# Performance work log

Measured on AMD Instinct MI355X. Metric: run time of the kernel, lower is better.

Reference implementation:

```python
import jax, jax.numpy as jnp
import numpy as np

B, S, HID = 1, 2048, 4096
NH, NKV, HD = 32, 8, 128
N_REP = NH // NKV
SCALING = HD ** -0.5
NEG_INF = jnp.float32(-jnp.inf)


def rotate_half(x):
    x1, x2 = jnp.split(x, 2, axis=-1)
    return jnp.concatenate((-x2, x1), axis=-1)


def setup_inputs() -> dict:
    key = jax.random.key(0)
    ks = jax.random.split(key, 8)
    hidden_states = jax.random.normal(ks[0], (B, S, HID), dtype=jnp.float32)
    # RoPE tables (uniform stand-ins; real cos/sin come from rotary embedding)
    pos = jnp.arange(S, dtype=jnp.float32)[:, None]
    inv_freq = 1.0 / (10000.0 ** (jnp.arange(0, HD, 2, dtype=jnp.float32) / HD))
    ang = pos * inv_freq[None, :]              # [S, HD/2]
    emb = jnp.concatenate([ang, ang], axis=-1)  # [S, HD]
    cos = jnp.cos(emb)[None].repeat(B, axis=0)  # [B, S, HD]
    sin = jnp.sin(emb)[None].repeat(B, axis=0)
    # HF-style additive causal mask: 0 on/below diagonal, -inf above
    tril = jnp.tril(jnp.ones((S, S), dtype=bool))
    attention_mask = jnp.where(tril, 0.0, NEG_INF).astype(jnp.float32)[None, None]  # [B,1,S,S]
    scale = 0.02
    q_w = jax.random.normal(ks[1], (HID, HID), dtype=jnp.float32) * scale
    k_w = jax.random.normal(ks[2], (NKV * HD, HID), dtype=jnp.float32) * scale
    v_w = jax.random.normal(ks[3], (NKV * HD, HID), dtype=jnp.float32) * scale
    o_w = jax.random.normal(ks[4], (HID, HID), dtype=jnp.float32) * scale
    return {"hidden_states": hidden_states, "cos": cos, "sin": sin,
            "attention_mask": attention_mask, "q_w": q_w, "k_w": k_w,
            "v_w": v_w, "o_w": o_w}


def reference(hidden_states, cos, sin, attention_mask, q_w, k_w, v_w, o_w):
    b, s, _ = hidden_states.shape
    # projections -> [B, H, S, D]
    q = (hidden_states @ q_w.T).reshape(b, s, NH, HD).transpose(0, 2, 1, 3)
    k = (hidden_states @ k_w.T).reshape(b, s, NKV, HD).transpose(0, 2, 1, 3)
    v = (hidden_states @ v_w.T).reshape(b, s, NKV, HD).transpose(0, 2, 1, 3)
    # RoPE (unsqueeze_dim=1)
    cos_u = cos[:, None, :, :]
    sin_u = sin[:, None, :, :]
    q = q * cos_u + rotate_half(q) * sin_u
    k = k * cos_u + rotate_half(k) * sin_u
    # repeat_kv (interleave each kv head n_rep times)
    k = jnp.repeat(k, N_REP, axis=1)
    v = jnp.repeat(v, N_REP, axis=1)
    attn = jnp.einsum("bhqd,bhkd->bhqk", q, k)
    # gen_mask: 0 -> 1, -inf -> 0 (passthrough otherwise)
    m = attention_mask
    mask01 = jnp.where(m == 0, 1.0, jnp.where(jnp.isneginf(m), 0.0, m))
    attn = attn * mask01
    causal = m[:, :, :, : k.shape[-2]]
    attn = (attn + causal) * SCALING
    probs = jax.nn.softmax(attn.astype(jnp.float32), axis=-1).astype(q.dtype)
    # dropout p=attention_dropout=0.0 in eval -> identity
    ctx = jnp.einsum("bhqk,bhkd->bhqd", probs, v)  # [B,H,S,D]
    out = ctx.transpose(0, 2, 1, 3).reshape(b, s, -1) @ o_w.T
    return out
```

## Files before the change

### kernel.cpp

```cpp
#include <hip/hip_runtime.h>


typedef __attribute__((ext_vector_type(8))) short bf16x8;
typedef __attribute__((ext_vector_type(4))) float f32x4;
typedef __attribute__((ext_vector_type(4))) unsigned short u16x4;

#define S_LEN 2048
#define HID 4096
#define NH 32
#define NKV 8
#define HD 128
#define KVDIM 1024
#define SCALING 0.08838834764831845f
#define ASC 0.12751744f
#define THR2 11.5415603f

__device__ inline unsigned short f2bf(float f) {
  unsigned u = __builtin_bit_cast(unsigned, f);
  u = (u + 0x7FFFu + ((u >> 16) & 1u)) >> 16;
  return (unsigned short)u;
}
__device__ inline unsigned short f2bf_fast(float f) {
  unsigned u = __builtin_bit_cast(unsigned, f);
  return (unsigned short)((u + 0x8000u) >> 16);
}
__device__ inline float bf2f(unsigned short h) {
  unsigned u = ((unsigned)h) << 16;
  return __builtin_bit_cast(float, u);
}

__device__ inline void gload_lds16(const unsigned short* g, unsigned short* l) {
  __builtin_amdgcn_global_load_lds(
      (const __attribute__((address_space(1))) void*)g,
      (__attribute__((address_space(3))) void*)l, 16, 0, 0);
}

#define SZ_HS (8388608u)
#define SZ_QW (16777216u)
#define SZ_KW (4194304u)
#define B0 SZ_HS
#define B1 (B0 + SZ_QW)
#define B2 (B1 + SZ_KW)
#define B3 (B2 + SZ_KW)
#define B4 (B3 + SZ_QW)

__global__ void cvt_all(const float* __restrict__ s0,
                        const float* __restrict__ s1,
                        const float* __restrict__ s2,
                        const float* __restrict__ s3,
                        const float* __restrict__ s4,
                        unsigned short* __restrict__ dst) {
  size_t i = ((size_t)blockIdx.x * blockDim.x + threadIdx.x) * 4;
  const float* src;
  size_t off;
  if (i < B0)      { src = s0; off = i; }
  else if (i < B1) { src = s1; off = i - B0; }
  else if (i < B2) { src = s2; off = i - B1; }
  else if (i < B3) { src = s3; off = i - B2; }
  else             { src = s4; off = i - B3; }
  f32x4 v = *(const f32x4*)(src + off);
  u16x4 o;
#pragma unroll
  for (int r = 0; r < 4; ++r) o[r] = f2bf(v[r]);
  *(u16x4*)(dst + i) = o;
}

__device__ inline const unsigned short* swz_src(const unsigned short* base,
                                                int s, int K) {
  const int g = s >> 3, q = s & 7, ls = q ^ (g & 7);
  return base + (size_t)(2 * g + (ls >> 2)) * K + (ls & 3) * 8;
}

__global__ __launch_bounds__(256, 3) void gemm_qkv(
    const unsigned short* __restrict__ A, const unsigned short* __restrict__ Bq_,
    const unsigned short* __restrict__ Bk_, const unsigned short* __restrict__ Bv_,
    const float* __restrict__ cosb, const float* __restrict__ sinb,
    unsigned short* __restrict__ Cq, unsigned short* __restrict__ Ck,
    unsigned short* __restrict__ Cvt) {
  __shared__ unsigned short As[2][128 * 32];
  __shared__ unsigned short Bs[2][128 * 32];
  const int K = HID;
  const int tid = threadIdx.x;
  const int lane = tid & 63;
  const int wave = tid >> 6;
  const int orig = blockIdx.y * gridDim.x + blockIdx.x;
  const int xcd = orig & 7, seq = orig >> 3;
  const int xt = xcd * ((int)gridDim.x >> 3) + (seq >> 4);
  const int yt = seq & 15;
  const int m0 = yt * 128;
  const int wr = wave >> 1, wc = wave & 1;
  const int lrow = lane & 15, lg = lane >> 4;

  const unsigned short* Bsel;
  if (xt < 32)      Bsel = Bq_ + (size_t)(xt * 128) * K;
  else if (xt < 40) Bsel = Bk_ + (size_t)((xt - 32) * 128) * K;
  else              Bsel = Bv_ + (size_t)((xt - 40) * 128) * K;

  const f32x4 zero = {0.f, 0.f, 0.f, 0.f};
  f32x4 acc[4][4];
#pragma unroll
  for (int i = 0; i < 4; ++i)
#pragma unroll
    for (int j = 0; j < 4; ++j) acc[i][j] = zero;

  const unsigned short* Ag0 = swz_src(A + (size_t)m0 * K, tid, K);
  const unsigned short* Ag1 = swz_src(A + (size_t)m0 * K, tid + 256, K);
  const unsigned short* Bg0 = swz_src(Bsel, tid, K);
  const unsigned short* Bg1 = swz_src(Bsel, tid + 256, K);
  unsigned short* Al0[2] = {&As[0][tid * 8], &As[1][tid * 8]};
  unsigned short* Al1[2] = {&As[0][(tid + 256) * 8], &As[1][(tid + 256) * 8]};
  unsigned short* Bl0[2] = {&Bs[0][tid * 8], &Bs[1][tid * 8]};
  unsigned short* Bl1[2] = {&Bs[0][(tid + 256) * 8], &Bs[1][(tid + 256) * 8]};

#define QKV_STAGE(buf, koff)                                                  \
  {                                                                           \
    gload_lds16(Ag0 + (koff), Al0[buf]);                                      \
    gload_lds16(Ag1 + (koff), Al1[buf]);                                      \
    gload_lds16(Bg0 + (koff), Bl0[buf]);                                      \
    gload_lds16(Bg1 + (koff), Bl1[buf]);                                      \
  }

  int colb[4];
#pragma unroll
  for (int j = 0; j < 4; ++j)
    colb[j] = wc * 32 + (j & 1) * 16 + (j >> 1) * 64;

  const int gl = lrow >> 1, p = lrow & 1;
  const int psw = gl * 64 + ((((p << 2) | lg) ^ (gl & 7)) << 3);

  QKV_STAGE(0, 0);
  __syncthreads();
  int cur = 0;
  const int NT = K >> 5;
  for (int kt = 0; kt < NT; ++kt) {
    if (kt + 1 < NT) QKV_STAGE(cur ^ 1, (kt + 1) * 32);
    bf16x8 af[4], bq[4];
#pragma unroll
    for (int i = 0; i < 4; ++i)
      af[i] = *(const bf16x8*)(&As[cur][(wr * 64 + i * 16) * 32 + psw]);
#pragma unroll
    for (int j = 0; j < 4; ++j)
      bq[j] = *(const bf16x8*)(&Bs[cur][colb[j] * 32 + psw]);
#pragma unroll
    for (int i = 0; i < 4; ++i)
#pragma unroll
      for (int j = 0; j < 4; ++j)
        acc[i][j] = __builtin_amdgcn_mfma_f32_16x16x32_bf16(af[i], bq[j],
                                                            acc[i][j], 0, 0, 0);
    __syncthreads();
    cur ^= 1;
  }
#undef QKV_STAGE

  if (xt < 40) {
    unsigned short* C = (xt < 32) ? Cq : Ck;
    const int ldc = (xt < 32) ? HID : KVDIM;
    const int n0 = (xt < 32) ? xt * 128 : (xt - 32) * 128;
#pragma unroll
    for (int i = 0; i < 4; ++i) {
#pragma unroll
      for (int jp = 0; jp < 2; ++jp) {
        const int d64 = wc * 32 + jp * 16 + lrow;
#pragma unroll
        for (int r = 0; r < 4; ++r) {
          const int s = m0 + wr * 64 + i * 16 + lg * 4 + r;
          const float cv = cosb[(size_t)s * 128 + d64];
          const float sv = sinb[(size_t)s * 128 + d64];
          const float lo = acc[i][jp][r], hi = acc[i][jp + 2][r];
          C[(size_t)s * ldc + n0 + d64]      = f2bf(lo * cv - hi * sv);
          C[(size_t)s * ldc + n0 + d64 + 64] = f2bf(hi * cv + lo * sv);
        }
      }
    }
  } else {
    const int n0 = (xt - 40) * 128;
#pragma unroll
    for (int i = 0; i < 4; ++i)
#pragma unroll
      for (int j = 0; j < 4; ++j) {
        const int mm = m0 + wr * 64 + i * 16 + lg * 4;
        const int nn = n0 + colb[j] + lrow;
        u16x4 pk;
#pragma unroll
        for (int r = 0; r < 4; ++r) pk[r] = f2bf(acc[i][j][r]);
        *(u16x4*)(Cvt + (size_t)nn * S_LEN + mm) = pk;
      }
  }
}

__global__ __launch_bounds__(256, 3) void gemm_o(
    const unsigned short* __restrict__ A, const unsigned short* __restrict__ B,
    float* __restrict__ C) {
  __shared__ unsigned short As[2][128 * 32];
  __shared__ unsigned short Bs[2][128 * 32];
  const int K = HID;
  const int tid = threadIdx.x;
  const int lane = tid & 63;
  const int wave = tid >> 6;
  const int orig = blockIdx.y * gridDim.x + blockIdx.x;
  const int xcd = orig & 7, seq = orig >> 3;
  const int xt = xcd * ((int)gridDim.x >> 3) + (seq >> 4);
  const int yt = seq & 15;
  const int m0 = yt * 128;
  const int n0 = xt * 128;
  const int wr = wave >> 1, wc = wave & 1;
  const int lrow = lane & 15, lg = lane >> 4;

  const f32x4 zero = {0.f, 0.f, 0.f, 0.f};
  f32x4 acc[4][4];
#pragma unroll
  for (int i = 0; i < 4; ++i)
#pragma unroll
    for (int j = 0; j < 4; ++j) acc[i][j] = zero;

  const unsigned short* Ag0 = swz_src(A + (size_t)m0 * K, tid, K);
  const unsigned short* Ag1 = swz_src(A + (size_t)m0 * K, tid + 256, K);
  const unsigned short* Bg0 = swz_src(B + (size_t)n0 * K, tid, K);
  const unsigned short* Bg1 = swz_src(B + (size_t)n0 * K, tid + 256, K);
  unsigned short* Al0[2] = {&As[0][tid * 8], &As[1][tid * 8]};
  unsigned short* Al1[2] = {&As[0][(tid + 256) * 8], &As[1][(tid + 256) * 8]};
  unsigned short* Bl0[2] = {&Bs[0][tid * 8], &Bs[1][tid * 8]};
  unsigned short* Bl1[2] = {&Bs[0][(tid + 256) * 8], &Bs[1][(tid + 256) * 8]};

#define O_STAGE(buf, koff)                                                    \
  {                                                                           \
    gload_lds16(Ag0 + (koff), Al0[buf]);                                      \
    gload_lds16(Ag1 + (koff), Al1[buf]);                                      \
    gload_lds16(Bg0 + (koff), Bl0[buf]);                                      \
    gload_lds16(Bg1 + (koff), Bl1[buf]);                                      \
  }

  const int gl = lrow >> 1, p = lrow & 1;
  const int psw = gl * 64 + ((((p << 2) | lg) ^ (gl & 7)) << 3);

  O_STAGE(0, 0);
  __syncthreads();
  int cur = 0;
  const int NT = K >> 5;
  for (int kt = 0; kt < NT; ++kt) {
    if (kt + 1 < NT) O_STAGE(cur ^ 1, (kt + 1) * 32);
    bf16x8 af[4], bq[4];
#pragma unroll
    for (int i = 0; i < 4; ++i) {
      af[i] = *(const bf16x8*)(&As[cur][(wr * 64 + i * 16) * 32 + psw]);
      bq[i] = *(const bf16x8*)(&Bs[cur][(wc * 64 + i * 16) * 32 + psw]);
    }
#pragma unroll
    for (int i = 0; i < 4; ++i)
#pragma unroll
      for (int j = 0; j < 4; ++j)
        acc[i][j] = __builtin_amdgcn_mfma_f32_16x16x32_bf16(af[i], bq[j],
                                                            acc[i][j], 0, 0, 0);
    __syncthreads();
    cur ^= 1;
  }
#undef O_STAGE

#pragma unroll
  for (int i = 0; i < 4; ++i)
#pragma unroll
    for (int j = 0; j < 4; ++j) {
      const int mm = m0 + wr * 64 + i * 16 + lg * 4;
      const int nn = n0 + wc * 64 + j * 16 + lrow;
#pragma unroll
      for (int r = 0; r < 4; ++r)
        C[(size_t)(mm + r) * HID + nn] = acc[i][j][r];
    }
}

__global__ __launch_bounds__(256, 2) void attn_kernel(
    const unsigned short* __restrict__ Q, const unsigned short* __restrict__ Kc,
    const unsigned short* __restrict__ Vt, unsigned short* __restrict__ ctx) {
  __shared__ unsigned short Ks[2][64 * 128];
  __shared__ unsigned short Vs[2][128 * 64];
  __shared__ unsigned short Ps[4][16 * 72];
  const int tid = threadIdx.x;
  const int lane = tid & 63;
  const int wave = tid >> 6;
  const int h = blockIdx.x;
  const int hk = h >> 2;
  const int yl = (int)gridDim.y - 1 - blockIdx.y;
  const int r0 = yl * 64 + wave * 16;
  const int lrow = lane & 15, lg = lane >> 4;

  bf16x8 aq[4];
  {
    const unsigned short* qb =
        Q + (size_t)(r0 + lrow) * HID + h * HD + lg * 8;
#pragma unroll
    for (int kk = 0; kk < 4; ++kk) aq[kk] = *(const bf16x8*)(qb + kk * 32);
  }

  const f32x4 zero = {0.f, 0.f, 0.f, 0.f};
  f32x4 o[8];
#pragma unroll
  for (int t = 0; t < 8; ++t) o[t] = zero;
  float l_i = 0.f;
  float m_i = -1e30f;

  const unsigned short* Kg[4];
  const unsigned short* Vg[4];
  int Koff[4], Voff[4];
#pragma unroll
  for (int qq = 0; qq < 4; ++qq) {
    const int slot = tid + 256 * qq;
    {
      const int row = slot >> 4, ch = slot & 15;
      Kg[qq] = Kc + (size_t)row * KVDIM + hk * HD + ((ch ^ (row & 7)) * 8);
      Koff[qq] = slot * 8;
    }
    {
      const int row = slot >> 3, ch = slot & 7;
      Vg[qq] = Vt + ((size_t)hk * HD + row) * S_LEN + ((ch ^ (row & 7)) * 8);
      Voff[qq] = slot * 8;
    }
  }
  unsigned short* pw = &Ps[wave][0];

#pragma unroll
  for (int qq = 0; qq < 4; ++qq) gload_lds16(Kg[qq], &Ks[0][Koff[qq]]);
#pragma unroll
  for (int qq = 0; qq < 4; ++qq) gload_lds16(Vg[qq], &Vs[0][Voff[qq]]);
  __syncthreads();

  const int NTk = yl + 1;
  for (int t = 0; t < NTk; ++t) {
    const int k0 = t << 6;
    const int cur = t & 1;
    const bool pf = (t + 1 < NTk);
    if (pf) {
#pragma unroll
      for (int qq = 0; qq < 4; ++qq)
        gload_lds16(Kg[qq] + (size_t)(k0 + 64) * KVDIM, &Ks[cur ^ 1][Koff[qq]]);
    }

    const bool compute = (k0 <= r0 + 15);
    f32x4 sacc[4];
    if (compute) {
#pragma unroll
      for (int c = 0; c < 4; ++c) sacc[c] = zero;
      __builtin_amdgcn_s_setprio(1);
#pragma unroll
      for (int c = 0; c < 4; ++c) {
        const int krow = c * 16 + lrow;
        bf16x8 bk[4];
#pragma unroll
        for (int kk = 0; kk < 4; ++kk)
          bk[kk] = *(const bf16x8*)(&Ks[cur][krow * 128 +
                                            (((kk * 4 + lg) ^ (krow & 7)) * 8)]);
#pragma unroll
        for (int kk = 0; kk < 4; ++kk)
          sacc[c] = __builtin_amdgcn_mfma_f32_16x16x32_bf16(
              bk[kk], aq[kk], sacc[c], 0, 0, 0);
      }
      __builtin_amdgcn_s_setprio(0);
    }
    if (pf) {
#pragma unroll
      for (int qq = 0; qq < 4; ++qq)
        gload_lds16(Vg[qq] + (k0 + 64), &Vs[cur ^ 1][Voff[qq]]);
    }
    if (compute) {
      const bool full = (k0 + 63 <= r0);
      const int q = r0 + lrow;
#pragma unroll
      for (int c = 0; c < 4; ++c)
#pragma unroll
        for (int r = 0; r < 4; ++r) {
          float v = sacc[c][r] * ASC;
          if (!full) {
            const int k = k0 + c * 16 + lg * 4 + r;
            v = (k <= q) ? v : -1e30f;
          }
          sacc[c][r] = v;
        }
      float m0v = fmaxf(fmaxf(sacc[0][0], sacc[0][1]),
                        fmaxf(sacc[0][2], sacc[0][3]));
      float m1v = fmaxf(fmaxf(sacc[1][0], sacc[1][1]),
                        fmaxf(sacc[1][2], sacc[1][3]));
      float m2v = fmaxf(fmaxf(sacc[2][0], sacc[2][1]),
                        fmaxf(sacc[2][2], sacc[2][3]));
      float m3v = fmaxf(fmaxf(sacc[3][0], sacc[3][1]),
                        fmaxf(sacc[3][2], sacc[3][3]));
      float tv = fmaxf(fmaxf(m0v, m1v), fmaxf(m2v, m3v));
      tv = fmaxf(tv, __shfl_xor(tv, 16, 64));
      tv = fmaxf(tv, __shfl_xor(tv, 32, 64));
      const float tm = tv;
      const bool grow = (tm > m_i + THR2);
      if (__any(grow)) {
        const float mn = fmaxf(m_i, tm);
        const float scq = __builtin_amdgcn_exp2f(m_i - mn);
        m_i = mn;
        l_i *= scq;
#pragma unroll
        for (int r = 0; r < 4; ++r) {
          const float scD = __shfl(scq, lg * 4 + r, 64);
#pragma unroll
          for (int t2 = 0; t2 < 8; ++t2) o[t2][r] *= scD;
        }
      }
      bf16x8 pa[2];
      {
        float rs = 0.f;
#pragma unroll
        for (int c = 0; c < 4; ++c) {
          u16x4 pk;
#pragma unroll
          for (int r = 0; r < 4; ++r) {
            const float p2 = __builtin_amdgcn_exp2f(sacc[c][r] - m_i);
            rs += p2;
            pk[r] = f2bf_fast(p2);
          }
          *(u16x4*)(pw + lrow * 72 + c * 16 + lg * 4) = pk;
        }
        rs += __shfl_xor(rs, 16, 64);
        rs += __shfl_xor(rs, 32, 64);
        l_i += rs;
#pragma unroll
        for (int ks = 0; ks < 2; ++ks)
          pa[ks] = *(const bf16x8*)(pw + lrow * 72 + ks * 32 + lg * 8);
      }
      __builtin_amdgcn_s_setprio(1);
#pragma unroll
      for (int t2 = 0; t2 < 8; ++t2) {
        const int vrow = t2 * 16 + lrow;
#pragma unroll
        for (int ks = 0; ks < 2; ++ks) {
          bf16x8 bv = *(const bf16x8*)(&Vs[cur][vrow * 64 +
                                               (((ks * 4 + lg) ^ (vrow & 7)) * 8)]);
          o[t2] = __builtin_amdgcn_mfma_f32_16x16x32_bf16(pa[ks], bv,
                                                          o[t2], 0, 0, 0);
        }
      }
      __builtin_amdgcn_s_setprio(0);
    }
    __syncthreads();
  }
  const float inv1 = 1.f / l_i;
#pragma unroll
  for (int r = 0; r < 4; ++r) {
    const float invD = __shfl(inv1, lg * 4 + r, 64);
#pragma unroll
    for (int t = 0; t < 8; ++t)
      ctx[(size_t)(r0 + lg * 4 + r) * HID + h * HD + t * 16 + lrow] =
          f2bf(o[t][r] * invD);
  }
}

extern "C" void kernel_launch(void* const* d_in, const int* in_sizes, int n_in,
                              void* d_out, int out_size, void* d_ws,
                              size_t ws_size, hipStream_t stream) {
  (void)in_sizes; (void)n_in; (void)out_size; (void)ws_size;
  const float* hs   = (const float*)d_in[0];
  const float* cosb = (const float*)d_in[1];
  const float* sinb = (const float*)d_in[2];
  const float* qw = (const float*)d_in[4];
  const float* kw = (const float*)d_in[5];
  const float* vw = (const float*)d_in[6];
  const float* ow = (const float*)d_in[7];
  float* out = (float*)d_out;

  unsigned short* ws = (unsigned short*)d_ws;
  unsigned short* hs_b = ws;
  unsigned short* qw_b = hs_b + SZ_HS;
  unsigned short* kw_b = qw_b + SZ_QW;
  unsigned short* vw_b = kw_b + SZ_KW;
  unsigned short* ow_b = vw_b + SZ_KW;
  unsigned short* q_b  = ow_b + SZ_QW;
  unsigned short* k_b  = q_b + SZ_HS;
  unsigned short* vt_b = k_b + (size_t)S_LEN * KVDIM;
  unsigned short* ctx_b = vt_b + (size_t)KVDIM * S_LEN;

  cvt_all<<<B4 / 1024, 256, 0, stream>>>(hs, qw, kw, vw, ow, hs_b);

  gemm_qkv<<<dim3(48, 16), 256, 0, stream>>>(hs_b, qw_b, kw_b, vw_b,
                                             cosb, sinb, q_b, k_b, vt_b);

  attn_kernel<<<dim3(NH, S_LEN / 64), 256, 0, stream>>>(q_b, k_b, vt_b, ctx_b);

  gemm_o<<<dim3(32, 16), 256, 0, stream>>>(ctx_b, ow_b, out);
}
```

Before: 326.3 us.

## Fuse fp32-to-bf16 weight conversion into GEMM B-tile loads

Removes the separate bulk conversion of all four weight matrices to bf16 and instead loads fp32 weight tiles directly inside the QKV and O GEMMs, converting in registers and writing bf16 to LDS after the MFMA block. The goal is to avoid the extra global write and re-read of ~40M weight elements. In exchange each GEMM reads twice as many bytes for B and loses async global-to-LDS loads for B, adding register pressure and VALU conversion work, and since weights are reused across 16 M-tiles each block converts redundantly.

```diff
diff --git a/kernel.cpp b/kernel.cpp
--- a/kernel.cpp
+++ b/kernel.cpp
@@ -38,31 +38,15 @@
 #define SZ_HS (8388608u)
 #define SZ_QW (16777216u)
 #define SZ_KW (4194304u)
-#define B0 SZ_HS
-#define B1 (B0 + SZ_QW)
-#define B2 (B1 + SZ_KW)
-#define B3 (B2 + SZ_KW)
-#define B4 (B3 + SZ_QW)
-
-__global__ void cvt_all(const float* __restrict__ s0,
-                        const float* __restrict__ s1,
-                        const float* __restrict__ s2,
-                        const float* __restrict__ s3,
-                        const float* __restrict__ s4,
-                        unsigned short* __restrict__ dst) {
+
+__global__ void cvt_hs(const float* __restrict__ in,
+                       unsigned short* __restrict__ out) {
   size_t i = ((size_t)blockIdx.x * blockDim.x + threadIdx.x) * 4;
-  const float* src;
-  size_t off;
-  if (i < B0)      { src = s0; off = i; }
-  else if (i < B1) { src = s1; off = i - B0; }
-  else if (i < B2) { src = s2; off = i - B1; }
-  else if (i < B3) { src = s3; off = i - B2; }
-  else             { src = s4; off = i - B3; }
-  f32x4 v = *(const f32x4*)(src + off);
+  f32x4 v = *(const f32x4*)(in + i);
   u16x4 o;
 #pragma unroll
   for (int r = 0; r < 4; ++r) o[r] = f2bf(v[r]);
-  *(u16x4*)(dst + i) = o;
+  *(u16x4*)(out + i) = o;
 }
 
 __device__ inline const unsigned short* swz_src(const unsigned short* base,
@@ -70,10 +54,14 @@
   const int g = s >> 3, q = s & 7, ls = q ^ (g & 7);
   return base + (size_t)(2 * g + (ls >> 2)) * K + (ls & 3) * 8;
 }
+__device__ inline const float* swz_srcf(const float* base, int s, int K) {
+  const int g = s >> 3, q = s & 7, ls = q ^ (g & 7);
+  return base + (size_t)(2 * g + (ls >> 2)) * K + (ls & 3) * 8;
+}
 
 __global__ __launch_bounds__(256, 3) void gemm_qkv(
-    const unsigned short* __restrict__ A, const unsigned short* __restrict__ Bq_,
-    const unsigned short* __restrict__ Bk_, const unsigned short* __restrict__ Bv_,
+    const unsigned short* __restrict__ A, const float* __restrict__ Bq_,
+    const float* __restrict__ Bk_, const float* __restrict__ Bv_,
     const float* __restrict__ cosb, const float* __restrict__ sinb,
     unsigned short* __restrict__ Cq, unsigned short* __restrict__ Ck,
     unsigned short* __restrict__ Cvt) {
@@ -91,10 +79,10 @@
   const int wr = wave >> 1, wc = wave & 1;
   const int lrow = lane & 15, lg = lane >> 4;
 
-  const unsigned short* Bsel;
-  if (xt < 32)      Bsel = Bq_ + (size_t)(xt * 128) * K;
-  else if (xt < 40) Bsel = Bk_ + (size_t)((xt - 32) * 128) * K;
-  else              Bsel = Bv_ + (size_t)((xt - 40) * 128) * K;
+  const float* Bself;
+  if (xt < 32)      Bself = Bq_ + (size_t)(xt * 128) * K;
+  else if (xt < 40) Bself = Bk_ + (size_t)((xt - 32) * 128) * K;
+  else              Bself = Bv_ + (size_t)((xt - 40) * 128) * K;
 
   const f32x4 zero = {0.f, 0.f, 0.f, 0.f};
   f32x4 acc[4][4];
@@ -105,19 +93,36 @@
 
   const unsigned short* Ag0 = swz_src(A + (size_t)m0 * K, tid, K);
   const unsigned short* Ag1 = swz_src(A + (size_t)m0 * K, tid + 256, K);
-  const unsigned short* Bg0 = swz_src(Bsel, tid, K);
-  const unsigned short* Bg1 = swz_src(Bsel, tid + 256, K);
+  const float* Bg0 = swz_srcf(Bself, tid, K);
+  const float* Bg1 = swz_srcf(Bself, tid + 256, K);
   unsigned short* Al0[2] = {&As[0][tid * 8], &As[1][tid * 8]};
   unsigned short* Al1[2] = {&As[0][(tid + 256) * 8], &As[1][(tid + 256) * 8]};
-  unsigned short* Bl0[2] = {&Bs[0][tid * 8], &Bs[1][tid * 8]};
-  unsigned short* Bl1[2] = {&Bs[0][(tid + 256) * 8], &Bs[1][(tid + 256) * 8]};
-
-#define QKV_STAGE(buf, koff)                                                  \
+
+  f32x4 bp00, bp01, bp10, bp11;
+
+#define QKV_ALOAD(buf, koff)                                                  \
   {                                                                           \
     gload_lds16(Ag0 + (koff), Al0[buf]);                                      \
     gload_lds16(Ag1 + (koff), Al1[buf]);                                      \
-    gload_lds16(Bg0 + (koff), Bl0[buf]);                                      \
-    gload_lds16(Bg1 + (koff), Bl1[buf]);                                      \
+  }
+#define QKV_BLOAD(koff)                                                       \
+  {                                                                           \
+    bp00 = *(const f32x4*)(Bg0 + (koff));                                     \
+    bp01 = *(const f32x4*)(Bg0 + (koff) + 4);                                 \
+    bp10 = *(const f32x4*)(Bg1 + (koff));                                     \
+    bp11 = *(const f32x4*)(Bg1 + (koff) + 4);                                 \
+  }
+#define QKV_BWRITE(buf)                                                       \
+  {                                                                           \
+    u16x4 w0, w1, w2, w3;                                                     \
+    _Pragma("unroll") for (int r = 0; r < 4; ++r) {                           \
+      w0[r] = f2bf(bp00[r]); w1[r] = f2bf(bp01[r]);                           \
+      w2[r] = f2bf(bp10[r]); w3[r] = f2bf(bp11[r]);                           \
+    }                                                                         \
+    *(u16x4*)&Bs[buf][tid * 8] = w0;                                          \
+    *(u16x4*)&Bs[buf][tid * 8 + 4] = w1;                                      \
+    *(u16x4*)&Bs[buf][(tid + 256) * 8] = w2;                                  \
+    *(u16x4*)&Bs[buf][(tid + 256) * 8 + 4] = w3;                              \
   }
 
   int colb[4];
@@ -128,12 +133,18 @@
   const int gl = lrow >> 1, p = lrow & 1;
   const int psw = gl * 64 + ((((p << 2) | lg) ^ (gl & 7)) << 3);
 
-  QKV_STAGE(0, 0);
+  QKV_ALOAD(0, 0);
+  QKV_BLOAD(0);
+  QKV_BWRITE(0);
   __syncthreads();
   int cur = 0;
   const int NT = K >> 5;
   for (int kt = 0; kt < NT; ++kt) {
-    if (kt + 1 < NT) QKV_STAGE(cur ^ 1, (kt + 1) * 32);
+    const bool pf = (kt + 1 < NT);
+    if (pf) {
+      QKV_ALOAD(cur ^ 1, (kt + 1) * 32);
+      QKV_BLOAD((kt + 1) * 32);
+    }
     bf16x8 af[4], bq[4];
 #pragma unroll
     for (int i = 0; i < 4; ++i)
@@ -147,10 +158,13 @@
       for (int j = 0; j < 4; ++j)
         acc[i][j] = __builtin_amdgcn_mfma_f32_16x16x32_bf16(af[i], bq[j],
                                                             acc[i][j], 0, 0, 0);
+    if (pf) QKV_BWRITE(cur ^ 1);
     __syncthreads();
     cur ^= 1;
   }
-#undef QKV_STAGE
+#undef QKV_ALOAD
+#undef QKV_BLOAD
+#undef QKV_BWRITE
 
   if (xt < 40) {
     unsigned short* C = (xt < 32) ? Cq : Ck;
@@ -189,7 +203,7 @@
 }
 
 __global__ __launch_bounds__(256, 3) void gemm_o(
-    const unsigned short* __restrict__ A, const unsigned short* __restrict__ B,
+    const unsigned short* __restrict__ A, const float* __restrict__ B,
     float* __restrict__ C) {
   __shared__ unsigned short As[2][128 * 32];
   __shared__ unsigned short Bs[2][128 * 32];
@@ -215,30 +229,53 @@
 
   const unsigned short* Ag0 = swz_src(A + (size_t)m0 * K, tid, K);
   const unsigned short* Ag1 = swz_src(A + (size_t)m0 * K, tid + 256, K);
-  const unsigned short* Bg0 = swz_src(B + (size_t)n0 * K, tid, K);
-  const unsigned short* Bg1 = swz_src(B + (size_t)n0 * K, tid + 256, K);
+  const float* Bg0 = swz_srcf(B + (size_t)n0 * K, tid, K);
+  const float* Bg1 = swz_srcf(B + (size_t)n0 * K, tid + 256, K);
   unsigned short* Al0[2] = {&As[0][tid * 8], &As[1][tid * 8]};
   unsigned short* Al1[2] = {&As[0][(tid + 256) * 8], &As[1][(tid + 256) * 8]};
-  unsigned short* Bl0[2] = {&Bs[0][tid * 8], &Bs[1][tid * 8]};
-  unsigned short* Bl1[2] = {&Bs[0][(tid + 256) * 8], &Bs[1][(tid + 256) * 8]};
-
-#define O_STAGE(buf, koff)                                                    \
+
+  f32x4 bp00, bp01, bp10, bp11;
+
+#define O_ALOAD(buf, koff)                                                    \
   {                                                                           \
     gload_lds16(Ag0 + (koff), Al0[buf]);                                      \
     gload_lds16(Ag1 + (koff), Al1[buf]);                                      \
-    gload_lds16(Bg0 + (koff), Bl0[buf]);                                      \
-    gload_lds16(Bg1 + (koff), Bl1[buf]);                                      \
+  }
+#define O_BLOAD(koff)                                                         \
+  {                                                                           \
+    bp00 = *(const f32x4*)(Bg0 + (koff));                                     \
+    bp01 = *(const f32x4*)(Bg0 + (koff) + 4);                                 \
+    bp10 = *(const f32x4*)(Bg1 + (koff));                                     \
+    bp11 = *(const f32x4*)(Bg1 + (koff) + 4);                                 \
+  }
+#define O_BWRITE(buf)                                                         \
+  {                                                                           \
+    u16x4 w0, w1, w2, w3;                                                     \
+    _Pragma("unroll") for (int r = 0; r < 4; ++r) {                           \
+      w0[r] = f2bf(bp00[r]); w1[r] = f2bf(bp01[r]);                           \
+      w2[r] = f2bf(bp10[r]); w3[r] = f2bf(bp11[r]);                           \
+    }                                                                         \
+    *(u16x4*)&Bs[buf][tid * 8] = w0;                                          \
+    *(u16x4*)&Bs[buf][tid * 8 + 4] = w1;                                      \
+    *(u16x4*)&Bs[buf][(tid + 256) * 8] = w2;                                  \
+    *(u16x4*)&Bs[buf][(tid + 256) * 8 + 4] = w3;                              \
   }
 
   const int gl = lrow >> 1, p = lrow & 1;
   const int psw = gl * 64 + ((((p << 2) | lg) ^ (gl & 7)) << 3);
 
-  O_STAGE(0, 0);
+  O_ALOAD(0, 0);
+  O_BLOAD(0);
+  O_BWRITE(0);
   __syncthreads();
   int cur = 0;
   const int NT = K >> 5;
   for (int kt = 0; kt < NT; ++kt) {
-    if (kt + 1 < NT) O_STAGE(cur ^ 1, (kt + 1) * 32);
+    const bool pf = (kt + 1 < NT);
+    if (pf) {
+      O_ALOAD(cur ^ 1, (kt + 1) * 32);
+      O_BLOAD((kt + 1) * 32);
+    }
     bf16x8 af[4], bq[4];
 #pragma unroll
     for (int i = 0; i < 4; ++i) {
@@ -251,10 +288,13 @@
       for (int j = 0; j < 4; ++j)
         acc[i][j] = __builtin_amdgcn_mfma_f32_16x16x32_bf16(af[i], bq[j],
                                                             acc[i][j], 0, 0, 0);
+    if (pf) O_BWRITE(cur ^ 1);
     __syncthreads();
     cur ^= 1;
   }
-#undef O_STAGE
+#undef O_ALOAD
+#undef O_BLOAD
+#undef O_BWRITE
 
 #pragma unroll
   for (int i = 0; i < 4; ++i)
@@ -462,21 +502,17 @@
 
   unsigned short* ws = (unsigned short*)d_ws;
   unsigned short* hs_b = ws;
-  unsigned short* qw_b = hs_b + SZ_HS;
-  unsigned short* kw_b = qw_b + SZ_QW;
-  unsigned short* vw_b = kw_b + SZ_KW;
-  unsigned short* ow_b = vw_b + SZ_KW;
-  unsigned short* q_b  = ow_b + SZ_QW;
+  unsigned short* q_b  = hs_b + SZ_HS;
   unsigned short* k_b  = q_b + SZ_HS;
   unsigned short* vt_b = k_b + (size_t)S_LEN * KVDIM;
   unsigned short* ctx_b = vt_b + (size_t)KVDIM * S_LEN;
 
-  cvt_all<<<B4 / 1024, 256, 0, stream>>>(hs, qw, kw, vw, ow, hs_b);
-
-  gemm_qkv<<<dim3(48, 16), 256, 0, stream>>>(hs_b, qw_b, kw_b, vw_b,
+  cvt_hs<<<SZ_HS / 1024, 256, 0, stream>>>(hs, hs_b);
+
+  gemm_qkv<<<dim3(48, 16), 256, 0, stream>>>(hs_b, qw, kw, vw,
                                              cosb, sinb, q_b, k_b, vt_b);
 
   attn_kernel<<<dim3(NH, S_LEN / 64), 256, 0, stream>>>(q_b, k_b, vt_b, ctx_b);
 
-  gemm_o<<<dim3(32, 16), 256, 0, stream>>>(ctx_b, ow_b, out);
-}
+  gemm_o<<<dim3(32, 16), 256, 0, stream>>>(ctx_b, ow, out);
+}
```

Measured after the change: 511.8 us. +56.9%, slower.
